# Optimization experiments

Hardware: AMD Instinct MI355X
Metric: run time of the kernel (lower is better)

Reference implementation:

```python
import jax, jax.numpy as jnp
import numpy as np

EPS = 1e-5
K = 20

def knn_idx(x, k):
    # x: (B, N, C) -> indices of k nearest neighbors (by negative squared distance, includes self)
    sq = jnp.sum(x * x, axis=-1)                                  # (B, N)
    d = 2.0 * jnp.einsum('bnc,bmc->bnm', x, x) - sq[:, :, None] - sq[:, None, :]
    return jax.lax.top_k(d, k)[1]                                 # (B, N, k)

def edge_conv(x, k, W, g, b, rm, rv):
    # x: (B, N, C); W: (O, 2C); BN params: (O,). Returns (B, N, O).
    idx = knn_idx(x, k)
    feat = jax.vmap(lambda xt, i: xt[i])(x, idx)                  # (B, N, k, C) neighbor gather
    ctr = jnp.broadcast_to(x[:, :, None, :], feat.shape)
    edge = jnp.concatenate([feat - ctr, ctr], axis=-1)            # (B, N, k, 2C)
    h = jnp.einsum('bnkc,oc->bnko', edge, W)                      # 1x1 conv
    h = g * (h - rm) * jax.lax.rsqrt(rv + EPS) + b                # BN (eval, running stats)
    h = jnp.where(h > 0, h, 0.2 * h)                              # LeakyReLU(0.2)
    return jnp.max(h, axis=2)                                     # max over k

def bn(h, g, b, rm, rv):
    return g * (h - rm) * jax.lax.rsqrt(rv + EPS) + b

def lrelu(h):
    return jnp.where(h > 0, h, 0.2 * h)

def _bn_params(key, c):
    k1, k2 = jax.random.split(key)
    g = 1.0 + 0.1 * jax.random.normal(k1, (c,), dtype=jnp.float32)
    b = 0.1 * jax.random.normal(k2, (c,), dtype=jnp.float32)
    return g, b, jnp.zeros((c,), jnp.float32), jnp.ones((c,), jnp.float32)

def setup_inputs() -> dict:
    key = jax.random.key(0)
    ks = jax.random.split(key, 16)
    B, Cin, N = 8, 6, 4096
    d = {'x': jax.random.normal(ks[0], (B, Cin, N), dtype=jnp.float32)}
    def w(k, o, i):
        return jax.random.normal(k, (o, i), dtype=jnp.float32) * (1.0 / np.sqrt(i))
    d['W1'] = w(ks[1], 64, 12);   d['g1'], d['b1'], d['m1'], d['v1'] = _bn_params(ks[2], 64)
    d['W2'] = w(ks[3], 64, 128);  d['g2'], d['b2'], d['m2'], d['v2'] = _bn_params(ks[4], 64)
    d['W3'] = w(ks[5], 128, 128); d['g3'], d['b3'], d['m3'], d['v3'] = _bn_params(ks[6], 128)
    d['W4'] = w(ks[7], 256, 256); d['g4'], d['b4'], d['m4'], d['v4'] = _bn_params(ks[8], 256)
    d['W5'] = w(ks[9], 1024, 512); d['g5'], d['b5'], d['m5'], d['v5'] = _bn_params(ks[10], 1024)
    d['L1'] = w(ks[11], 512, 2048); d['gl1'], d['bl1'], d['ml1'], d['vl1'] = _bn_params(ks[12], 512)
    d['L2'] = w(ks[13], 256, 512); d['L2b'] = jnp.zeros((256,), jnp.float32)
    d['gl2'], d['bl2'], d['ml2'], d['vl2'] = _bn_params(ks[14], 256)
    d['L3'] = w(ks[15], 2, 256);  d['L3b'] = jnp.zeros((2,), jnp.float32)
    return d

def reference(x, W1, g1, b1, m1, v1, W2, g2, b2, m2, v2, W3, g3, b3, m3, v3,
              W4, g4, b4, m4, v4, W5, g5, b5, m5, v5,
              L1, gl1, bl1, ml1, vl1, L2, L2b, gl2, bl2, ml2, vl2, L3, L3b):
    xt = jnp.transpose(x, (0, 2, 1))                              # (B, N, 6)
    x1 = edge_conv(xt, K, W1, g1, b1, m1, v1)                     # (B, N, 64)
    x2 = edge_conv(x1, K, W2, g2, b2, m2, v2)                     # (B, N, 64)
    x3 = edge_conv(x2, K, W3, g3, b3, m3, v3)                     # (B, N, 128)
    x4 = edge_conv(x3, K, W4, g4, b4, m4, v4)                     # (B, N, 256)
    xc = jnp.concatenate([x1, x2, x3, x4], axis=-1)               # (B, N, 512)
    h = lrelu(bn(jnp.einsum('bnc,oc->bno', xc, W5), g5, b5, m5, v5))  # (B, N, 1024)
    pooled = jnp.concatenate([jnp.max(h, axis=1), jnp.mean(h, axis=1)], axis=-1)  # (B, 2048)
    o = lrelu(bn(pooled @ L1.T, gl1, bl1, ml1, vl1))
    o = lrelu(bn(o @ L2.T + L2b, gl2, bl2, ml2, vl2))
    return o @ L3.T + L3b                                         # (B, 2)
```

## Files before the change

### kernel.cpp

```cpp
#include <hip/hip_runtime.h>


#define NPTS   4096
#define NB     8
#define BNR    32768
#define KNN    20
#define EPSBN  1e-5f

__device__ __forceinline__ float lrelu(float x){ return x > 0.f ? x : 0.2f*x; }

__global__ __launch_bounds__(256) void k_transpose_pad(const float* __restrict__ x,
                                                       float* __restrict__ xt){
  int id = blockIdx.x*256 + threadIdx.x;
  int b = id >> 12, n = id & (NPTS-1);
  const float* xb = x + (size_t)b*6*NPTS + n;
  float* o = xt + (size_t)id*8;
#pragma unroll
  for (int c = 0; c < 6; ++c) o[c] = xb[(size_t)c*NPTS];
  o[6] = 0.f; o[7] = 0.f;
}

__global__ __launch_bounds__(256) void k_sqnorm(const float* __restrict__ X, int xstride, int c4,
                                                float* __restrict__ sq){
  int id = blockIdx.x*256 + threadIdx.x;
  const float4* r = (const float4*)(X + (size_t)id*xstride);
  float s = 0.f;
  for (int c = 0; c < c4; ++c){ float4 v = r[c]; s += v.x*v.x + v.y*v.y + v.z*v.z + v.w*v.w; }
  sq[id] = s;
}

__global__ __launch_bounds__(256) void k_dgemm(const float* __restrict__ X, int xstride, int Kdim,
                                               const float* __restrict__ sqv,
                                               float* __restrict__ D){
  __shared__ float As[16][136];
  __shared__ float Bs[16][136];
  const int i0 = blockIdx.y*128, j0 = blockIdx.x*128;
  const int tid = threadIdx.x, tx = tid & 15, ty = tid >> 4;
  float acc[8][8] = {};
  for (int k0 = 0; k0 < Kdim; k0 += 16){
#pragma unroll
    for (int i = 0; i < 8; ++i){
      int li = tid + 256*i;
      int row = li >> 4, kk = li & 15;
      bool ok = (k0 + kk) < Kdim;
      As[kk][row] = ok ? X[(size_t)(i0+row)*xstride + k0+kk] : 0.f;
      Bs[kk][row] = ok ? X[(size_t)(j0+row)*xstride + k0+kk] : 0.f;
    }
    __syncthreads();
#pragma unroll
    for (int kk = 0; kk < 16; ++kk){
      float a[8], b[8];
      *(float4*)&a[0] = *(const float4*)&As[kk][ty*8];
      *(float4*)&a[4] = *(const float4*)&As[kk][ty*8+4];
      *(float4*)&b[0] = *(const float4*)&Bs[kk][tx*8];
      *(float4*)&b[4] = *(const float4*)&Bs[kk][tx*8+4];
#pragma unroll
      for (int r = 0; r < 8; ++r)
#pragma unroll
        for (int c = 0; c < 8; ++c)
          acc[r][c] = fmaf(a[r], b[c], acc[r][c]);
    }
    __syncthreads();
  }
  float sj[8];
#pragma unroll
  for (int c = 0; c < 8; ++c) sj[c] = sqv[j0 + tx*8 + c];
#pragma unroll
  for (int r = 0; r < 8; ++r){
    int irow = i0 + ty*8 + r;
    float si = sqv[irow];
    float* drow = D + (size_t)irow*NPTS + j0 + tx*8;
    float4 v0 = make_float4(2.f*acc[r][0]-si-sj[0], 2.f*acc[r][1]-si-sj[1],
                            2.f*acc[r][2]-si-sj[2], 2.f*acc[r][3]-si-sj[3]);
    float4 v1 = make_float4(2.f*acc[r][4]-si-sj[4], 2.f*acc[r][5]-si-sj[5],
                            2.f*acc[r][6]-si-sj[6], 2.f*acc[r][7]-si-sj[7]);
    *(float4*)&drow[0] = v0;
    *(float4*)&drow[4] = v1;
  }
}

__global__ __launch_bounds__(256) void k_scan(const float* __restrict__ D,
                                              int* __restrict__ idx){
  const int lane = threadIdx.x & 63;
  const int wv   = threadIdx.x >> 6;
  const int row  = blockIdx.x*4 + wv;
  const float* drow = D + (size_t)row*NPTS;
  float bv = -1e30f; int bi = -1;
  float thr = -1e30f;
  float dcur = drow[lane];
  for (int m0 = 0; m0 < NPTS; m0 += 64){
    float dnext = (m0 + 64 < NPTS) ? drow[m0 + 64 + lane] : -1e30f;
    unsigned long long mask = __ballot(dcur > thr);
    while (mask){
      int l = __ffsll(mask) - 1;
      mask &= mask - 1;
      float dv = __shfl(dcur, l);
      if (dv > thr){
        float upv = __shfl_up(bv, 1);
        int   upi = __shfl_up(bi, 1);
        if (lane < KNN){
          bool ins  = dv > bv;
          bool insp = (lane > 0) && (dv > upv);
          if (ins){ bv = insp ? upv : dv; bi = insp ? upi : (m0 + l); }
        }
        thr = __shfl(bv, KNN-1);
      }
    }
    dcur = dnext;
  }
  if (lane < KNN) idx[(size_t)row*KNN + lane] = bi;
}

__global__ __launch_bounds__(256) void k_gemm_xw(const float* __restrict__ X, int xstride, int Kdim,
                                                 const float* __restrict__ W, int wstride,
                                                 float* __restrict__ Out, int ostride){
  __shared__ float Xs[16][68];
  __shared__ float Ws[16][68];
  const int m0 = blockIdx.x*64, o0 = blockIdx.y*64;
  const int tid = threadIdx.x, tx = tid & 15, ty = tid >> 4;
  float acc[4][4] = {};
  for (int k0 = 0; k0 < Kdim; k0 += 16){
#pragma unroll
    for (int i = 0; i < 4; ++i){
      int li = tid + 256*i;
      int row = li >> 4, kk = li & 15;
      bool ok = (k0 + kk) < Kdim;
      Xs[kk][row] = ok ? X[(size_t)(m0+row)*xstride + k0+kk] : 0.f;
      Ws[kk][row] = ok ? W[(size_t)(o0+row)*wstride + k0+kk] : 0.f;
    }
    __syncthreads();
#pragma unroll
    for (int kk = 0; kk < 16; ++kk){
      float xa[4], wb[4];
      *(float4*)xa = *(const float4*)&Xs[kk][ty*4];
      *(float4*)wb = *(const float4*)&Ws[kk][tx*4];
#pragma unroll
      for (int i = 0; i < 4; ++i)
#pragma unroll
        for (int j = 0; j < 4; ++j)
          acc[i][j] = fmaf(xa[i], wb[j], acc[i][j]);
    }
    __syncthreads();
  }
#pragma unroll
  for (int i = 0; i < 4; ++i){
    float4 v = make_float4(acc[i][0], acc[i][1], acc[i][2], acc[i][3]);
    *(float4*)&Out[(size_t)(m0+ty*4+i)*ostride + o0 + tx*4] = v;
  }
}

__global__ __launch_bounds__(256) void k_gather_conv(const float* __restrict__ P,
                                                     const float* __restrict__ Q,
                                                     const int* __restrict__ idx,
                                                     const float* __restrict__ g,
                                                     const float* __restrict__ bb,
                                                     const float* __restrict__ rm,
                                                     const float* __restrict__ rv,
                                                     float* __restrict__ Out, int oshift, int choff){
  const int O = 1 << oshift;
  int id = blockIdx.x*256 + threadIdx.x;
  int gn = id >> oshift;
  int o  = id & (O-1);
  int bbase = (gn >> 12) * NPTS;
  const int* ip = idx + (size_t)gn*KNN;
  float vmax = -1e30f, vmin = 1e30f;
#pragma unroll
  for (int k = 0; k < KNN; ++k){
    int m = ip[k];
    float v = P[((size_t)(bbase + m) << oshift) + o];
    vmax = fmaxf(vmax, v);
    vmin = fminf(vmin, v);
  }
  float scale = g[o] * rsqrtf(rv[o] + EPSBN);
  float beta  = bb[o] - rm[o]*scale;
  float R = (scale >= 0.f) ? vmax : vmin;
  float h = R - P[((size_t)gn << oshift) + o] + Q[((size_t)gn << oshift) + o];
  Out[(size_t)gn*512 + choff + o] = lrelu(fmaf(scale, h, beta));
}

__global__ __launch_bounds__(256) void k_gemm_w5_pool(const float* __restrict__ X,
                                                      const float* __restrict__ W,
                                                      const float* __restrict__ g,
                                                      const float* __restrict__ bb,
                                                      const float* __restrict__ rm,
                                                      const float* __restrict__ rv,
                                                      float* __restrict__ pmax,
                                                      float* __restrict__ psum){
  __shared__ float Xs[16][136];
  __shared__ float Ws[16][136];
  __shared__ float red[2][16][128];
  const int m0 = blockIdx.x*128, o0 = blockIdx.y*128;
  const int tid = threadIdx.x, tx = tid & 15, ty = tid >> 4;
  float acc[8][8] = {};
  for (int k0 = 0; k0 < 512; k0 += 16){
#pragma unroll
    for (int i = 0; i < 8; ++i){
      int li = tid + 256*i;
      int row = li >> 4, kk = li & 15;
      Xs[kk][row] = X[(size_t)(m0+row)*512 + k0+kk];
      Ws[kk][row] = W[(size_t)(o0+row)*512 + k0+kk];
    }
    __syncthreads();
#pragma unroll
    for (int kk = 0; kk < 16; ++kk){
      float xa[8], wb[8];
      *(float4*)&xa[0] = *(const float4*)&Xs[kk][ty*8];
      *(float4*)&xa[4] = *(const float4*)&Xs[kk][ty*8+4];
      *(float4*)&wb[0] = *(const float4*)&Ws[kk][tx*8];
      *(float4*)&wb[4] = *(const float4*)&Ws[kk][tx*8+4];
#pragma unroll
      for (int i = 0; i < 8; ++i)
#pragma unroll
        for (int j = 0; j < 8; ++j)
          acc[i][j] = fmaf(xa[i], wb[j], acc[i][j]);
    }
    __syncthreads();
  }
#pragma unroll
  for (int j = 0; j < 8; ++j){
    int o = o0 + tx*8 + j;
    float scale = g[o] * rsqrtf(rv[o] + EPSBN);
    float beta  = bb[o] - rm[o]*scale;
    float mx = -1e30f, sm = 0.f;
#pragma unroll
    for (int i = 0; i < 8; ++i){
      float h = lrelu(fmaf(scale, acc[i][j], beta));
      mx = fmaxf(mx, h);
      sm += h;
    }
    red[0][ty][tx*8+j] = mx;
    red[1][ty][tx*8+j] = sm;
  }
  __syncthreads();
  if (tid < 128){
    float mx = -1e30f, sm = 0.f;
#pragma unroll
    for (int t = 0; t < 16; ++t){
      mx = fmaxf(mx, red[0][t][tid]);
      sm += red[1][t][tid];
    }
    pmax[(size_t)blockIdx.x*1024 + o0 + tid] = mx;
    psum[(size_t)blockIdx.x*1024 + o0 + tid] = sm;
  }
}

__global__ __launch_bounds__(256) void k_pool_reduce(const float* __restrict__ pmax,
                                                     const float* __restrict__ psum,
                                                     float* __restrict__ pooled){
  int id = blockIdx.x*256 + threadIdx.x;
  int b = id >> 10, o = id & 1023;
  float mx = -1e30f, sm = 0.f;
  for (int t = 0; t < 32; ++t){
    mx = fmaxf(mx, pmax[(size_t)(b*32+t)*1024 + o]);
    sm += psum[(size_t)(b*32+t)*1024 + o];
  }
  pooled[(size_t)b*2048 + o] = mx;
  pooled[(size_t)b*2048 + 1024 + o] = sm * (1.f/NPTS);
}

__global__ __launch_bounds__(256) void k_fc1(const float* __restrict__ pooled,
                                             const float* __restrict__ W,
                                             const float* __restrict__ g,
                                             const float* __restrict__ bb,
                                             const float* __restrict__ rm,
                                             const float* __restrict__ rv,
                                             float* __restrict__ out){
  __shared__ float4 xs[512];
  int b = blockIdx.x >> 1;
  int o = ((blockIdx.x & 1) << 8) + threadIdx.x;
  const float4* pr = (const float4*)(pooled + (size_t)b*2048);
  for (int l = threadIdx.x; l < 512; l += 256) xs[l] = pr[l];
  __syncthreads();
  const float4* wr = (const float4*)(W + (size_t)o*2048);
  float s0=0.f, s1=0.f, s2=0.f, s3=0.f;
#pragma unroll 4
  for (int c = 0; c < 512; ++c){
    float4 w = wr[c], v = xs[c];
    s0 = fmaf(v.x, w.x, s0); s1 = fmaf(v.y, w.y, s1);
    s2 = fmaf(v.z, w.z, s2); s3 = fmaf(v.w, w.w, s3);
  }
  float h = (s0+s1)+(s2+s3);
  float scale = g[o] * rsqrtf(rv[o] + EPSBN);
  float beta  = bb[o] - rm[o]*scale;
  out[(size_t)b*512 + o] = lrelu(fmaf(scale, h, beta));
}

__global__ __launch_bounds__(256) void k_fc2(const float* __restrict__ in,
                                             const float* __restrict__ W,
                                             const float* __restrict__ bias,
                                             const float* __restrict__ g,
                                             const float* __restrict__ bb,
                                             const float* __restrict__ rm,
                                             const float* __restrict__ rv,
                                             float* __restrict__ out){
  __shared__ float4 xs[128];
  int b = blockIdx.x;
  int o = threadIdx.x;
  const float4* pr = (const float4*)(in + (size_t)b*512);
  if (threadIdx.x < 128) xs[threadIdx.x] = pr[threadIdx.x];
  __syncthreads();
  const float4* wr = (const float4*)(W + (size_t)o*512);
  float s0=0.f, s1=0.f, s2=0.f, s3=0.f;
#pragma unroll 4
  for (int c = 0; c < 128; ++c){
    float4 w = wr[c], v = xs[c];
    s0 = fmaf(v.x, w.x, s0); s1 = fmaf(v.y, w.y, s1);
    s2 = fmaf(v.z, w.z, s2); s3 = fmaf(v.w, w.w, s3);
  }
  float h = (s0+s1)+(s2+s3) + bias[o];
  float scale = g[o] * rsqrtf(rv[o] + EPSBN);
  float beta  = bb[o] - rm[o]*scale;
  out[(size_t)b*256 + o] = lrelu(fmaf(scale, h, beta));
}

__global__ __launch_bounds__(64) void k_fc3(const float* __restrict__ in,
                                            const float* __restrict__ W,
                                            const float* __restrict__ bias,
                                            float* __restrict__ out){
  int t = threadIdx.x;
  if (t >= 16) return;
  int b = t >> 1, o = t & 1;
  const float* xr = in + (size_t)b*256;
  const float* wr = W + (size_t)o*256;
  float s = 0.f;
  for (int c = 0; c < 256; ++c) s = fmaf(xr[c], wr[c], s);
  out[b*2 + o] = s + bias[o];
}

extern "C" void kernel_launch(void* const* d_in, const int* in_sizes, int n_in,
                              void* d_out, int out_size, void* d_ws, size_t ws_size,
                              hipStream_t stream){
  (void)in_sizes; (void)n_in; (void)out_size;
  const float* x   = (const float*)d_in[0];
  const float* W1  = (const float*)d_in[1];
  const float* g1  = (const float*)d_in[2];
  const float* b1  = (const float*)d_in[3];
  const float* m1  = (const float*)d_in[4];
  const float* v1  = (const float*)d_in[5];
  const float* W2  = (const float*)d_in[6];
  const float* g2  = (const float*)d_in[7];
  const float* b2  = (const float*)d_in[8];
  const float* m2  = (const float*)d_in[9];
  const float* v2  = (const float*)d_in[10];
  const float* W3  = (const float*)d_in[11];
  const float* g3  = (const float*)d_in[12];
  const float* b3  = (const float*)d_in[13];
  const float* m3  = (const float*)d_in[14];
  const float* v3  = (const float*)d_in[15];
  const float* W4  = (const float*)d_in[16];
  const float* g4  = (const float*)d_in[17];
  const float* b4  = (const float*)d_in[18];
  const float* m4  = (const float*)d_in[19];
  const float* v4  = (const float*)d_in[20];
  const float* W5  = (const float*)d_in[21];
  const float* g5  = (const float*)d_in[22];
  const float* b5  = (const float*)d_in[23];
  const float* m5  = (const float*)d_in[24];
  const float* v5  = (const float*)d_in[25];
  const float* L1  = (const float*)d_in[26];
  const float* gl1 = (const float*)d_in[27];
  const float* bl1 = (const float*)d_in[28];
  const float* ml1 = (const float*)d_in[29];
  const float* vl1 = (const float*)d_in[30];
  const float* L2  = (const float*)d_in[31];
  const float* L2b = (const float*)d_in[32];
  const float* gl2 = (const float*)d_in[33];
  const float* bl2 = (const float*)d_in[34];
  const float* ml2 = (const float*)d_in[35];
  const float* vl2 = (const float*)d_in[36];
  const float* L3  = (const float*)d_in[37];
  const float* L3b = (const float*)d_in[38];

  float* ws   = (float*)d_ws;
  float* xt   = ws;
  float* sq   = ws + 262144;
  int*   idx  = (int*)(ws + 294912);
  float* Dbuf = ws + 950272;
  float* P    = Dbuf;
  float* Q    = Dbuf + 8388608;
  float* xc   = ws + 17727488;
  float* pmax = ws + 34504704;
  float* psum = ws + 34766848;
  float* pool = ws + 35028992;
  float* oA   = ws + 35045376;
  float* oB   = ws + 35049472;
  if (ws_size < (size_t)35051520 * 4) return;

  k_transpose_pad<<<128, 256, 0, stream>>>(x, xt);

  k_sqnorm<<<128, 256, 0, stream>>>(xt, 8, 2, sq);
  for (int b = 0; b < NB; ++b){
    k_dgemm<<<dim3(32,32), 256, 0, stream>>>(xt + (size_t)b*NPTS*8, 8, 8, sq + b*NPTS, Dbuf);
    k_scan<<<1024, 256, 0, stream>>>(Dbuf, idx + (size_t)b*NPTS*KNN);
  }
  k_gemm_xw<<<dim3(512,1), 256, 0, stream>>>(xt, 8, 6, W1,     12, P, 64);
  k_gemm_xw<<<dim3(512,1), 256, 0, stream>>>(xt, 8, 6, W1 + 6, 12, Q, 64);
  k_gather_conv<<<8192, 256, 0, stream>>>(P, Q, idx, g1, b1, m1, v1, xc, 6, 0);

  k_sqnorm<<<128, 256, 0, stream>>>(xc, 512, 16, sq);
  for (int b = 0; b < NB; ++b){
    k_dgemm<<<dim3(32,32), 256, 0, stream>>>(xc + (size_t)b*NPTS*512, 512, 64, sq + b*NPTS, Dbuf);
    k_scan<<<1024, 256, 0, stream>>>(Dbuf, idx + (size_t)b*NPTS*KNN);
  }
  k_gemm_xw<<<dim3(512,1), 256, 0, stream>>>(xc, 512, 64, W2,      128, P, 64);
  k_gemm_xw<<<dim3(512,1), 256, 0, stream>>>(xc, 512, 64, W2 + 64, 128, Q, 64);
  k_gather_conv<<<8192, 256, 0, stream>>>(P, Q, idx, g2, b2, m2, v2, xc, 6, 64);

  k_sqnorm<<<128, 256, 0, stream>>>(xc + 64, 512, 16, sq);
  for (int b = 0; b < NB; ++b){
    k_dgemm<<<dim3(32,32), 256, 0, stream>>>(xc + 64 + (size_t)b*NPTS*512, 512, 64, sq + b*NPTS, Dbuf);
    k_scan<<<1024, 256, 0, stream>>>(Dbuf, idx + (size_t)b*NPTS*KNN);
  }
  k_gemm_xw<<<dim3(512,2), 256, 0, stream>>>(xc + 64, 512, 64, W3,      128, P, 128);
  k_gemm_xw<<<dim3(512,2), 256, 0, stream>>>(xc + 64, 512, 64, W3 + 64, 128, Q, 128);
  k_gather_conv<<<16384, 256, 0, stream>>>(P, Q, idx, g3, b3, m3, v3, xc, 7, 128);

  k_sqnorm<<<128, 256, 0, stream>>>(xc + 128, 512, 32, sq);
  for (int b = 0; b < NB; ++b){
    k_dgemm<<<dim3(32,32), 256, 0, stream>>>(xc + 128 + (size_t)b*NPTS*512, 512, 128, sq + b*NPTS, Dbuf);
    k_scan<<<1024, 256, 0, stream>>>(Dbuf, idx + (size_t)b*NPTS*KNN);
  }
  k_gemm_xw<<<dim3(512,4), 256, 0, stream>>>(xc + 128, 512, 128, W4,       256, P, 256);
  k_gemm_xw<<<dim3(512,4), 256, 0, stream>>>(xc + 128, 512, 128, W4 + 128, 256, Q, 256);
  k_gather_conv<<<32768, 256, 0, stream>>>(P, Q, idx, g4, b4, m4, v4, xc, 8, 256);

  k_gemm_w5_pool<<<dim3(256,8), 256, 0, stream>>>(xc, W5, g5, b5, m5, v5, pmax, psum);
  k_pool_reduce<<<32, 256, 0, stream>>>(pmax, psum, pool);

  k_fc1<<<16, 256, 0, stream>>>(pool, L1, gl1, bl1, ml1, vl1, oA);
  k_fc2<<<8, 256, 0, stream>>>(oA, L2, L2b, gl2, bl2, ml2, vl2, oB);
  k_fc3<<<1, 64, 0, stream>>>(oB, L3, L3b, (float*)d_out);
}
```

Before: 3.459 ms.

## Exploit distance-matrix symmetry and remap GEMM B-fragment to cut LDS bank conflicts

```diff
diff --git a/kernel.cpp b/kernel.cpp
--- a/kernel.cpp
+++ b/kernel.cpp
@@ -32,9 +32,11 @@
 __global__ __launch_bounds__(256) void k_dgemm(const float* __restrict__ X, int xstride, int Kdim,
                                                const float* __restrict__ sqv,
                                                float* __restrict__ D){
-  __shared__ float As[16][136];
-  __shared__ float Bs[16][136];
-  const int i0 = blockIdx.y*128, j0 = blockIdx.x*128;
+  const int bi = blockIdx.y, bj = blockIdx.x;
+  if (bj < bi) return;
+  __shared__ float As[16][132];
+  __shared__ float Bs[16][132];
+  const int i0 = bi*128, j0 = bj*128;
   const int tid = threadIdx.x, tx = tid & 15, ty = tid >> 4;
   float acc[8][8] = {};
   for (int k0 = 0; k0 < Kdim; k0 += 16){
@@ -52,8 +54,8 @@
       float a[8], b[8];
       *(float4*)&a[0] = *(const float4*)&As[kk][ty*8];
       *(float4*)&a[4] = *(const float4*)&As[kk][ty*8+4];
-      *(float4*)&b[0] = *(const float4*)&Bs[kk][tx*8];
-      *(float4*)&b[4] = *(const float4*)&Bs[kk][tx*8+4];
+      *(float4*)&b[0] = *(const float4*)&Bs[kk][tx*4];
+      *(float4*)&b[4] = *(const float4*)&Bs[kk][64 + tx*4];
 #pragma unroll
       for (int r = 0; r < 8; ++r)
 #pragma unroll
@@ -64,18 +66,34 @@
   }
   float sj[8];
 #pragma unroll
-  for (int c = 0; c < 8; ++c) sj[c] = sqv[j0 + tx*8 + c];
+  for (int c = 0; c < 4; ++c){
+    sj[c]   = sqv[j0 + tx*4 + c];
+    sj[c+4] = sqv[j0 + 64 + tx*4 + c];
+  }
+  float si[8];
+#pragma unroll
+  for (int r = 0; r < 8; ++r) si[r] = sqv[i0 + ty*8 + r];
+#pragma unroll
+  for (int r = 0; r < 8; ++r)
+#pragma unroll
+    for (int c = 0; c < 8; ++c)
+      acc[r][c] = 2.f*acc[r][c] - si[r] - sj[c];
 #pragma unroll
   for (int r = 0; r < 8; ++r){
-    int irow = i0 + ty*8 + r;
-    float si = sqv[irow];
-    float* drow = D + (size_t)irow*NPTS + j0 + tx*8;
-    float4 v0 = make_float4(2.f*acc[r][0]-si-sj[0], 2.f*acc[r][1]-si-sj[1],
-                            2.f*acc[r][2]-si-sj[2], 2.f*acc[r][3]-si-sj[3]);
-    float4 v1 = make_float4(2.f*acc[r][4]-si-sj[4], 2.f*acc[r][5]-si-sj[5],
-                            2.f*acc[r][6]-si-sj[6], 2.f*acc[r][7]-si-sj[7]);
-    *(float4*)&drow[0] = v0;
-    *(float4*)&drow[4] = v1;
+    float* drow = D + (size_t)(i0 + ty*8 + r)*NPTS;
+    *(float4*)&drow[j0 + tx*4]      = make_float4(acc[r][0], acc[r][1], acc[r][2], acc[r][3]);
+    *(float4*)&drow[j0 + 64 + tx*4] = make_float4(acc[r][4], acc[r][5], acc[r][6], acc[r][7]);
+  }
+  if (bj > bi){
+#pragma unroll
+    for (int c = 0; c < 4; ++c){
+      float* drow0 = D + (size_t)(j0 + tx*4 + c)*NPTS + i0 + ty*8;
+      *(float4*)&drow0[0] = make_float4(acc[0][c], acc[1][c], acc[2][c], acc[3][c]);
+      *(float4*)&drow0[4] = make_float4(acc[4][c], acc[5][c], acc[6][c], acc[7][c]);
+      float* drow1 = D + (size_t)(j0 + 64 + tx*4 + c)*NPTS + i0 + ty*8;
+      *(float4*)&drow1[0] = make_float4(acc[0][c+4], acc[1][c+4], acc[2][c+4], acc[3][c+4]);
+      *(float4*)&drow1[4] = make_float4(acc[4][c+4], acc[5][c+4], acc[6][c+4], acc[7][c+4]);
+    }
   }
 }
 
@@ -186,8 +204,8 @@
                                                       const float* __restrict__ rv,
                                                       float* __restrict__ pmax,
                                                       float* __restrict__ psum){
-  __shared__ float Xs[16][136];
-  __shared__ float Ws[16][136];
+  __shared__ float Xs[16][132];
+  __shared__ float Ws[16][132];
   __shared__ float red[2][16][128];
   const int m0 = blockIdx.x*128, o0 = blockIdx.y*128;
   const int tid = threadIdx.x, tx = tid & 15, ty = tid >> 4;
@@ -206,8 +224,8 @@
       float xa[8], wb[8];
       *(float4*)&xa[0] = *(const float4*)&Xs[kk][ty*8];
       *(float4*)&xa[4] = *(const float4*)&Xs[kk][ty*8+4];
-      *(float4*)&wb[0] = *(const float4*)&Ws[kk][tx*8];
-      *(float4*)&wb[4] = *(const float4*)&Ws[kk][tx*8+4];
+      *(float4*)&wb[0] = *(const float4*)&Ws[kk][tx*4];
+      *(float4*)&wb[4] = *(const float4*)&Ws[kk][64 + tx*4];
 #pragma unroll
       for (int i = 0; i < 8; ++i)
 #pragma unroll
@@ -218,7 +236,8 @@
   }
 #pragma unroll
   for (int j = 0; j < 8; ++j){
-    int o = o0 + tx*8 + j;
+    int ocol = (j < 4) ? (tx*4 + j) : (64 + tx*4 + j - 4);
+    int o = o0 + ocol;
     float scale = g[o] * rsqrtf(rv[o] + EPSBN);
     float beta  = bb[o] - rm[o]*scale;
     float mx = -1e30f, sm = 0.f;
@@ -228,8 +247,8 @@
       mx = fmaxf(mx, h);
       sm += h;
     }
-    red[0][ty][tx*8+j] = mx;
-    red[1][ty][tx*8+j] = sm;
+    red[0][ty][ocol] = mx;
+    red[1][ty][ocol] = sm;
   }
   __syncthreads();
   if (tid < 128){
@@ -366,8 +385,8 @@
   const float* L2b = (const float*)d_in[32];
   const float* gl2 = (const float*)d_in[33];
   const float* bl2 = (const float*)d_in[34];
+  const float* vl2_g = (const float*)d_in[36];
   const float* ml2 = (const float*)d_in[35];
-  const float* vl2 = (const float*)d_in[36];
   const float* L3  = (const float*)d_in[37];
   const float* L3b = (const float*)d_in[38];
 
@@ -428,6 +447,6 @@
   k_pool_reduce<<<32, 256, 0, stream>>>(pmax, psum, pool);
 
   k_fc1<<<16, 256, 0, stream>>>(pool, L1, gl1, bl1, ml1, vl1, oA);
-  k_fc2<<<8, 256, 0, stream>>>(oA, L2, L2b, gl2, bl2, ml2, vl2, oB);
+  k_fc2<<<8, 256, 0, stream>>>(oA, L2, L2b, gl2, bl2, ml2, vl2_g, oB);
   k_fc3<<<1, 64, 0, stream>>>(oB, L3, L3b, (float*)d_out);
 }
```

Result: slower. 3.577 ms (+3.4%).
